# Kernel tuning notes

Hardware: AMD Instinct MI355X
Metric: run time of the kernel (lower is better)

The kernel has to match this reference:

```python
import jax, jax.numpy as jnp
import numpy as np

G = 8          # GroupNorm groups
EPS = 1e-5
L = 4          # num_layers
C = 64         # hidden_channels
CIN = 2        # in_channels


def group_norm(x, gamma, beta):
    B, Cc, H, W = x.shape
    xr = x.reshape(B, G, Cc // G, H, W)
    mu = xr.mean(axis=(2, 3, 4), keepdims=True)
    var = xr.var(axis=(2, 3, 4), keepdims=True)
    xn = ((xr - mu) * jax.lax.rsqrt(var + EPS)).reshape(B, Cc, H, W)
    return xn * gamma[:, None, None] + beta[:, None, None]


def conv1x1(x, w, b):
    # x: [B,Ci,H,W], w: [Co,Ci] -> [B,Co,H,W]
    return jnp.einsum('bchw,oc->bohw', x, w) + b[None, :, None, None]


def conv3x3(x, w, b):
    y = jax.lax.conv_general_dilated(x, w, (1, 1), 'SAME',
                                     dimension_numbers=('NCHW', 'OIHW', 'NCHW'))
    return y + b[None, :, None, None]


def setup_inputs() -> dict:
    key = jax.random.key(0)
    ks = jax.random.split(key, 20)
    s = 0.05
    inp = {
        'x': jax.random.normal(ks[0], (2, CIN, 256, 256), jnp.float32),
        'hidden': jnp.zeros((2, L, C, C), jnp.float32),
        'W_in': jax.random.normal(ks[1], (C, CIN, 3, 3), jnp.float32) * s,
        'b_in': jnp.zeros((C,), jnp.float32),
        'gamma': jnp.ones((L, C), jnp.float32),
        'beta': jnp.zeros((L, C), jnp.float32),
        'Wq': jax.random.normal(ks[2], (L, C, C), jnp.float32) * s,
        'bq': jnp.zeros((L, C), jnp.float32),
        'Wk': jax.random.normal(ks[3], (L, C, C), jnp.float32) * s,
        'bk': jnp.zeros((L, C), jnp.float32),
        'Wv': jax.random.normal(ks[4], (L, C, C), jnp.float32) * s,
        'bv': jnp.zeros((L, C), jnp.float32),
        'Wg': jax.random.normal(ks[5], (L, 2 * C, C), jnp.float32) * s,
        'bg': jnp.zeros((L, 2 * C), jnp.float32),
        'Wp': jax.random.normal(ks[6], (L, C, C), jnp.float32) * s,
        'bp': jnp.zeros((L, C), jnp.float32),
        'W_out': jax.random.normal(ks[7], (CIN, C, 3, 3), jnp.float32) * s,
        'b_out': jnp.zeros((CIN,), jnp.float32),
    }
    return inp


def gla_layer(feat, prev_mem, gamma, beta, Wq, bq, Wk, bk, Wv, bv, Wg, bg, Wp, bp):
    B, Cc, H, W = feat.shape
    N = H * W
    scale = Cc ** (-0.5)
    xn = group_norm(feat, gamma, beta)
    q = conv1x1(xn, Wq, bq).reshape(B, Cc, N) * scale
    k = conv1x1(xn, Wk, bk).reshape(B, Cc, N)
    v = conv1x1(xn, Wv, bv).reshape(B, Cc, N)
    gates = conv1x1(xn, Wg, bg).reshape(B, 2 * Cc, N)
    f_gate = jax.nn.sigmoid(gates[:, :Cc])
    i_gate = jax.nn.sigmoid(gates[:, Cc:])
    k_gated = k * i_gate
    new_knowledge = jnp.einsum('bcn,bdn->bcd', k_gated, v) / N  # [B,C,C]
    global_forget = f_gate.mean(axis=2)[:, :, None]              # [B,C,1]
    new_mem = global_forget * prev_mem + new_knowledge
    retrieved = jnp.einsum('bcn,bcd->bdn', q, new_mem).reshape(B, Cc, H, W)
    out = conv1x1(retrieved, Wp, bp) + feat
    return out, new_mem


def reference(x, hidden, W_in, b_in, gamma, beta, Wq, bq, Wk, bk, Wv, bv,
              Wg, bg, Wp, bp, W_out, b_out):
    feat = conv3x3(x, W_in, b_in)
    mems = []
    for i in range(L):
        feat, m = gla_layer(feat, hidden[:, i], gamma[i], beta[i],
                            Wq[i], bq[i], Wk[i], bk[i], Wv[i], bv[i],
                            Wg[i], bg[i], Wp[i], bp[i])
        mems.append(m)
    new_hidden = jnp.stack(mems, axis=1)  # [B,L,C,C]
    out = conv3x3(feat, W_out, b_out) + x
    return out, new_hidden
```

## Files before the change

### kernel.cpp

```cpp
#include <hip/hip_runtime.h>
#include <hip/hip_bf16.h>

typedef __hip_bfloat16 bf16;
typedef __attribute__((ext_vector_type(8))) short bf16x8;
typedef __attribute__((ext_vector_type(4))) short short4v;
typedef __attribute__((ext_vector_type(4))) float f32x4;

#define BATCH 2
#define CH 64
#define NPIX 65536
#define HDIM 256
#define NLAYER 4
#define NGRP 8
#define NSLOT 512

#define OFS_FEAT   0ull
#define OFS_KSLOT  16777216ull
#define OFS_MEMBG  25165824ull
#define OFS_FSUM   25182208ull
#define OFS_SSUM   25198592ull
#define OFS_BEFF   25214976ull
#define OFS_MEFFB  25215488ull
#define OFS_WKB    25231872ull
#define OFS_WVB    25264640ull
#define OFS_WGB    25297408ull
#define OFS_WTOUT  25362944ull
#define OFS_WPB    25367552ull
#define OFS_WQTB   25400320ull
#define ZERO_BYTES 32768

__device__ __forceinline__ float sigmoidf_(float x){ return 1.0f/(1.0f+__expf(-x)); }

__device__ __forceinline__ short f2bs(float x){
  unsigned u = __float_as_uint(x);
  u += 0x7fffu + ((u >> 16) & 1u);
  return (short)(u >> 16);
}
__device__ __forceinline__ float bs2f(short x){
  return __uint_as_float(((unsigned)(unsigned short)x) << 16);
}

__device__ __forceinline__ float waveReduce(float v){
  #pragma unroll
  for (int off=32; off; off>>=1) v += __shfl_xor(v, off, 64);
  return v;
}

__global__ void k_prepw(const float* __restrict__ Wk, const float* __restrict__ Wv,
                        const float* __restrict__ Wg, const float* __restrict__ Wout,
                        const float* __restrict__ Wp, const float* __restrict__ Wq,
                        short* __restrict__ Wkb, short* __restrict__ Wvb,
                        short* __restrict__ Wgb, float* __restrict__ wtout,
                        short* __restrict__ Wpb, short* __restrict__ Wqtb){
  int i = blockIdx.x*256 + threadIdx.x;
  if (i < 16384){
    Wkb[i] = f2bs(Wk[i]);
    Wvb[i] = f2bs(Wv[i]);
    Wpb[i] = f2bs(Wp[i]);
    int l = i >> 12, within = i & 4095;
    int e = within >> 6, c = within & 63;
    Wqtb[i] = f2bs(Wq[l*4096 + c*64 + e]);
  }
  if (i < 32768) Wgb[i] = f2bs(Wg[i]);
  if (i < 1152){
    int o = i / 576, rem = i % 576;
    int k = rem >> 6, c = rem & 63;
    wtout[(o*9 + k)*64 + c] = Wout[o*576 + c*9 + k];
  }
}

__device__ __forceinline__ void blockStats(const float* gs, const float* gq,
                                           float* ssum_b, int t){
  __shared__ float sacc[16];
  if (t < 16) sacc[t] = 0.f;
  __syncthreads();
  #pragma unroll
  for (int g=0; g<NGRP; g++){
    float s  = waveReduce(gs[g]);
    float sq = waveReduce(gq[g]);
    if ((t & 63) == 0){ atomicAdd(&sacc[g*2], s); atomicAdd(&sacc[g*2+1], sq); }
  }
  __syncthreads();
  if (t < 16) atomicAdd(&ssum_b[t*32], sacc[t]);
}

__global__ void k_conv_in(const float* __restrict__ x, const float* __restrict__ w,
                          const float* __restrict__ bias,
                          short* __restrict__ feat, float* __restrict__ ssum){
  int b = blockIdx.y;
  int t = threadIdx.x;
  int n = blockIdx.x*256 + t;
  int y = n >> 8, xx = n & 255;
  float patch[18];
  int idx = 0;
  #pragma unroll
  for (int ci=0; ci<2; ci++)
    #pragma unroll
    for (int dy=-1; dy<=1; dy++)
      #pragma unroll
      for (int dx=-1; dx<=1; dx++){
        int yy = y+dy, xc = xx+dx;
        float v = 0.f;
        if (yy>=0 && yy<HDIM && xc>=0 && xc<HDIM)
          v = x[((b*2+ci)*HDIM + yy)*HDIM + xc];
        patch[idx++] = v;
      }
  float gs[NGRP], gq[NGRP];
  #pragma unroll
  for (int g=0; g<NGRP; g++){ gs[g]=0.f; gq[g]=0.f; }
  short* fb = feat + ((size_t)b*NPIX + n)*64;
  #pragma unroll
  for (int c4=0; c4<16; c4++){
    short4v sv;
    #pragma unroll
    for (int j=0;j<4;j++){
      int o = c4*4 + j;
      float acc = bias[o];
      #pragma unroll
      for (int k=0; k<18; k++) acc += w[o*18+k]*patch[k];
      sv[j] = f2bs(acc);
      gs[o>>3] += acc; gq[o>>3] += acc*acc;
    }
    *(short4v*)(fb + c4*4) = sv;
  }
  blockStats(gs, gq, ssum + b*512, t);
}

__device__ __forceinline__ void gnCoef(const float* __restrict__ ssum_l, int b, int t,
                                       const float* __restrict__ gammaP,
                                       const float* __restrict__ betaP, int l,
                                       float* s_gnA, float* s_gnB){
  if (t < 64){
    int g = t >> 3;
    const float inv = 1.0f/(8.0f*NPIX);
    float s  = ssum_l[(b*16 + g*2)*32];
    float sq = ssum_l[(b*16 + g*2 + 1)*32];
    float mu = s*inv;
    float var = sq*inv - mu*mu;
    float rstd = rsqrtf(var + 1e-5f);
    float A = rstd * gammaP[l*64 + t];
    s_gnA[t] = A;
    s_gnB[t] = betaP[l*64 + t] - mu * A;
  }
}

__global__ __launch_bounds__(256,3) void k_qkvg_know(
    const short* __restrict__ feat, const float* __restrict__ ssum_l,
    const float* __restrict__ gammaP, const float* __restrict__ betaP,
    const short* __restrict__ Wkb, const float* __restrict__ bkP,
    const short* __restrict__ Wvb, const float* __restrict__ bvP,
    const short* __restrict__ Wgb, const float* __restrict__ bgP,
    int l, short* __restrict__ kslot, float* __restrict__ f_sum)
{
  int b = blockIdx.y;
  int n0 = blockIdx.x * 128;
  int t = threadIdx.x;
  int w = t >> 6;
  int lane = t & 63;
  int m = lane & 15;
  int quad = lane >> 4;
  int rowbase = w*16;

  __shared__ short s_buf[17408];
  short* s_kg = s_buf;
  short* s_v  = s_buf + 8704;
  short* s_xn = s_buf;
  __shared__ float s_gnA[64], s_gnB[64];

  gnCoef(ssum_l, b, t, gammaP, betaP, l, s_gnA, s_gnB);

  float bkv[4], biv[4], bvv[4], bfv[4], fs[4];
  #pragma unroll
  for (int r=0;r<4;r++){
    int row = rowbase + quad*4 + r;
    bkv[r] = bkP[l*64 + row];
    biv[r] = bgP[l*128 + 64 + row];
    bvv[r] = bvP[l*64 + row];
    bfv[r] = bgP[l*128 + row];
    fs[r] = 0.f;
  }
  f32x4 z4 = {0.f,0.f,0.f,0.f};
  f32x4 accn[4];
  #pragma unroll
  for (int dt=0;dt<4;dt++) accn[dt] = z4;

  __syncthreads();

  const short* fbase = feat + ((size_t)b*NPIX + n0)*64;
  #pragma unroll
  for (int i=0;i<4;i++){
    int chunk = t + i*256;
    int px = chunk >> 3, c8 = (chunk & 7)*8;
    bf16x8 rv = *(const bf16x8*)(fbase + px*64 + c8);
    short4v lo, hi;
    #pragma unroll
    for (int j=0;j<4;j++)
      lo[j] = f2bs(fmaf(bs2f(rv[j]), s_gnA[c8+j], s_gnB[c8+j]));
    #pragma unroll
    for (int j=0;j<4;j++)
      hi[j] = f2bs(fmaf(bs2f(rv[j+4]), s_gnA[c8+4+j], s_gnB[c8+4+j]));
    *(short4v*)&s_xn[px*72 + c8]     = lo;
    *(short4v*)&s_xn[px*72 + c8 + 4] = hi;
  }
  __syncthreads();

  bf16x8 Bf[2][8];
  #pragma unroll
  for (int kc=0;kc<2;kc++)
    #pragma unroll
    for (int nt=0;nt<8;nt++)
      Bf[kc][nt] = *(const bf16x8*)&s_xn[(nt*16+m)*72 + kc*32 + quad*8];
  __syncthreads();

  {
    bf16x8 Ak[2], Ai[2];
    #pragma unroll
    for (int kc=0;kc<2;kc++){
      Ak[kc] = *(const bf16x8*)&Wkb[l*4096 + (rowbase+m)*64 + kc*32 + quad*8];
      Ai[kc] = *(const bf16x8*)&Wgb[l*8192 + (64+rowbase+m)*64 + kc*32 + quad*8];
    }
    #pragma unroll
    for (int half=0; half<2; half++){
      f32x4 acck[4], acci[4];
      #pragma unroll
      for (int q4=0;q4<4;q4++){ acck[q4]=z4; acci[q4]=z4; }
      #pragma unroll
      for (int kc=0;kc<2;kc++)
        #pragma unroll
        for (int q4=0;q4<4;q4++){
          acck[q4] = __builtin_amdgcn_mfma_f32_16x16x32_bf16(Ak[kc], Bf[kc][half*4+q4], acck[q4], 0,0,0);
          acci[q4] = __builtin_amdgcn_mfma_f32_16x16x32_bf16(Ai[kc], Bf[kc][half*4+q4], acci[q4], 0,0,0);
        }
      #pragma unroll
      for (int q4=0;q4<4;q4++){
        int nt = half*4+q4;
        #pragma unroll
        for (int r=0;r<4;r++){
          int row = rowbase + quad*4 + r;
          float kv = acck[q4][r] + bkv[r];
          float iv = acci[q4][r] + biv[r];
          s_kg[row*136 + nt*16 + m] = f2bs(kv * sigmoidf_(iv));
        }
      }
    }
  }
  {
    bf16x8 Av[2];
    #pragma unroll
    for (int kc=0;kc<2;kc++)
      Av[kc] = *(const bf16x8*)&Wvb[l*4096 + (rowbase+m)*64 + kc*32 + quad*8];
    #pragma unroll
    for (int half=0; half<2; half++){
      f32x4 accv[4];
      #pragma unroll
      for (int q4=0;q4<4;q4++) accv[q4]=z4;
      #pragma unroll
      for (int kc=0;kc<2;kc++)
        #pragma unroll
        for (int q4=0;q4<4;q4++)
          accv[q4] = __builtin_amdgcn_mfma_f32_16x16x32_bf16(Av[kc], Bf[kc][half*4+q4], accv[q4], 0,0,0);
      #pragma unroll
      for (int q4=0;q4<4;q4++){
        int nt = half*4+q4;
        #pragma unroll
        for (int r=0;r<4;r++){
          int row = rowbase + quad*4 + r;
          s_v[row*136 + nt*16 + m] = f2bs(accv[q4][r] + bvv[r]);
        }
      }
    }
  }
  {
    bf16x8 Af[2];
    #pragma unroll
    for (int kc=0;kc<2;kc++)
      Af[kc] = *(const bf16x8*)&Wgb[l*8192 + (rowbase+m)*64 + kc*32 + quad*8];
    #pragma unroll
    for (int half=0; half<2; half++){
      f32x4 accf[4];
      #pragma unroll
      for (int q4=0;q4<4;q4++) accf[q4]=z4;
      #pragma unroll
      for (int kc=0;kc<2;kc++)
        #pragma unroll
        for (int q4=0;q4<4;q4++)
          accf[q4] = __builtin_amdgcn_mfma_f32_16x16x32_bf16(Af[kc], Bf[kc][half*4+q4], accf[q4], 0,0,0);
      #pragma unroll
      for (int q4=0;q4<4;q4++)
        #pragma unroll
        for (int r=0;r<4;r++)
          fs[r] += sigmoidf_(accf[q4][r] + bfv[r]);
    }
  }
  __syncthreads();

  #pragma unroll
  for (int kc4=0; kc4<4; kc4++){
    bf16x8 a = *(const bf16x8*)&s_kg[(rowbase + m)*136 + kc4*32 + quad*8];
    #pragma unroll
    for (int dt=0; dt<4; dt++){
      bf16x8 bv8 = *(const bf16x8*)&s_v[(dt*16 + m)*136 + kc4*32 + quad*8];
      accn[dt] = __builtin_amdgcn_mfma_f32_16x16x32_bf16(a, bv8, accn[dt], 0,0,0);
    }
  }

  #pragma unroll
  for (int off=1; off<16; off<<=1)
    #pragma unroll
    for (int r=0;r<4;r++) fs[r] += __shfl_xor(fs[r], off, 64);
  if (m == 0){
    #pragma unroll
    for (int r=0;r<4;r++)
      atomicAdd(&f_sum[(b*64 + rowbase + quad*4 + r)*32], fs[r]);
  }
  short* kr = kslot + ((size_t)b*NSLOT + blockIdx.x)*4096;
  #pragma unroll
  for (int dt=0;dt<4;dt++)
    #pragma unroll
    for (int r=0;r<4;r++)
      kr[(rowbase + quad*4 + r)*64 + dt*16 + m] = f2bs(accn[dt][r]);
}

__global__ __launch_bounds__(256) void k_memreduce(
    const short* __restrict__ kslot, const float* __restrict__ f_sum,
    const float* __restrict__ hidden_in, int l,
    float* __restrict__ hidden_out, short* __restrict__ membG)
{
  int b = blockIdx.y;
  int t = threadIdx.x;
  int e = t & 127;
  int half = t >> 7;
  int cd = blockIdx.x*128 + e;

  const short* base = kslot + ((size_t)b*NSLOT + half*256)*4096 + cd;
  float s = 0.f;
  #pragma unroll 16
  for (int sl=0; sl<256; sl++) s += bs2f(base[(size_t)sl*4096]);

  __shared__ float red[128];
  if (half) red[e] = s;
  __syncthreads();
  if (!half){
    const float invN = 1.0f/(float)NPIX;
    float kn = (s + red[e]) * invN;
    float fmean = f_sum[(b*64 + (cd>>6))*32] * invN;
    float pm = hidden_in[(size_t)(b*NLAYER+l)*4096 + cd];
    float nm = fmean*pm + kn;
    hidden_out[(size_t)(b*NLAYER+l)*4096 + cd] = nm;
    membG[b*4096 + cd] = f2bs(nm);
  }
}

__global__ __launch_bounds__(256) void k_meff(
    const short* __restrict__ membG, float* __restrict__ f_sum,
    const short* __restrict__ Wpb, const short* __restrict__ Wqtb,
    const float* __restrict__ bqP, const float* __restrict__ bpP,
    int l, short* __restrict__ Meffb, float* __restrict__ beff,
    float* __restrict__ ssum_next)
{
  int b = blockIdx.x;
  int t = threadIdx.x;
  int w = t >> 6;
  int lane = t & 63;
  int m = lane & 15;
  int quad = lane >> 4;

  __shared__ short s_memb[64*72];
  __shared__ short s_mfb[64*72];
  __shared__ float s_bq[64];

  if (t < 64) s_bq[t] = bqP[l*64 + t];

  #pragma unroll
  for (int i=0;i<16;i++){
    int cd = t + i*256;
    int c = cd >> 6, d = cd & 63;
    s_memb[c*72 + d] = membG[b*4096 + cd];
  }
  __syncthreads();
  if (t < 64) f_sum[(b*64 + t)*32] = 0.f;
  if (t < 16) ssum_next[(b*16 + t)*32] = 0.f;

  f32x4 z4 = {0.f,0.f,0.f,0.f};

  bf16x8 Ap[2];
  #pragma unroll
  for (int kc=0;kc<2;kc++)
    Ap[kc] = *(const bf16x8*)&Wpb[l*4096 + (w*16+m)*64 + kc*32 + quad*8];

  float be[4];
  #pragma unroll
  for (int r=0;r<4;r++) be[r] = 0.f;

  #pragma unroll
  for (int ct=0; ct<4; ct++){
    f32x4 a = z4;
    #pragma unroll
    for (int kc=0;kc<2;kc++){
      bf16x8 Bm = *(const bf16x8*)&s_memb[(ct*16+m)*72 + kc*32 + quad*8];
      a = __builtin_amdgcn_mfma_f32_16x16x32_bf16(Ap[kc], Bm, a, 0,0,0);
    }
    int c = ct*16 + m;
    #pragma unroll
    for (int r=0;r<4;r++){
      int o = w*16 + quad*4 + r;
      s_mfb[o*72 + c] = f2bs(a[r]);
      be[r] += a[r] * s_bq[c];
    }
  }
  #pragma unroll
  for (int off=1; off<16; off<<=1)
    #pragma unroll
    for (int r=0;r<4;r++) be[r] += __shfl_xor(be[r], off, 64);
  if (m == 0){
    #pragma unroll
    for (int r=0;r<4;r++){
      int o = w*16 + quad*4 + r;
      beff[b*64 + o] = bpP[l*64 + o] + 0.125f*be[r];
    }
  }
  __syncthreads();

  bf16x8 Am2[2];
  #pragma unroll
  for (int kc=0;kc<2;kc++)
    Am2[kc] = *(const bf16x8*)&s_mfb[(w*16+m)*72 + kc*32 + quad*8];
  #pragma unroll
  for (int et=0; et<4; et++){
    f32x4 a = z4;
    #pragma unroll
    for (int kc=0;kc<2;kc++){
      bf16x8 Bq = *(const bf16x8*)&Wqtb[l*4096 + (et*16+m)*64 + kc*32 + quad*8];
      a = __builtin_amdgcn_mfma_f32_16x16x32_bf16(Am2[kc], Bq, a, 0,0,0);
    }
    #pragma unroll
    for (int r=0;r<4;r++){
      int o = w*16 + quad*4 + r;
      Meffb[(size_t)b*4096 + o*64 + et*16 + m] = f2bs(0.125f*a[r]);
    }
  }
}

__global__ __launch_bounds__(256,3) void k_retrproj(
    const float* __restrict__ ssum_l,
    const float* __restrict__ gammaP, const float* __restrict__ betaP,
    const short* __restrict__ Meffb, const float* __restrict__ beff,
    int l, short* __restrict__ feat, float* __restrict__ ssum_next)
{
  int b = blockIdx.y;
  int n0 = blockIdx.x * 128;
  int t = threadIdx.x;
  int w = t >> 6;
  int lane = t & 63;
  int m = lane & 15;
  int quad = lane >> 4;

  __shared__ float s_out[128*68];
  short* s_xn = (short*)s_out;
  __shared__ float s_gnA[64], s_gnB[64], s_beff[64];
  __shared__ float s_sacc[16];

  gnCoef(ssum_l, b, t, gammaP, betaP, l, s_gnA, s_gnB);
  if (t < 64) s_beff[t] = beff[b*64 + t];
  if (t < 16) s_sacc[t] = 0.f;
  __syncthreads();

  short* fbase = feat + ((size_t)b*NPIX + n0)*64;
  #pragma unroll
  for (int i=0;i<4;i++){
    int chunk = t + i*256;
    int px = chunk >> 3, c8 = (chunk & 7)*8;
    bf16x8 rv = *(const bf16x8*)(fbase + px*64 + c8);
    short4v lo, hi;
    #pragma unroll
    for (int j=0;j<4;j++)
      lo[j] = f2bs(fmaf(bs2f(rv[j]), s_gnA[c8+j], s_gnB[c8+j]));
    #pragma unroll
    for (int j=0;j<4;j++)
      hi[j] = f2bs(fmaf(bs2f(rv[j+4]), s_gnA[c8+4+j], s_gnB[c8+4+j]));
    *(short4v*)&s_xn[px*72 + c8]     = lo;
    *(short4v*)&s_xn[px*72 + c8 + 4] = hi;
  }
  __syncthreads();

  bf16x8 Bf[2][8];
  #pragma unroll
  for (int kc=0;kc<2;kc++)
    #pragma unroll
    for (int nt=0;nt<8;nt++)
      Bf[kc][nt] = *(const bf16x8*)&s_xn[(nt*16+m)*72 + kc*32 + quad*8];

  bf16x8 Am[2];
  #pragma unroll
  for (int kc=0;kc<2;kc++)
    Am[kc] = *(const bf16x8*)&Meffb[(size_t)b*4096 + (w*16 + m)*64 + kc*32 + quad*8];
  __syncthreads();

  f32x4 acc[8];
  f32x4 z4 = {0.f,0.f,0.f,0.f};
  #pragma unroll
  for (int nt=0;nt<8;nt++) acc[nt]=z4;
  #pragma unroll
  for (int kc=0;kc<2;kc++)
    #pragma unroll
    for (int nt=0;nt<8;nt++)
      acc[nt] = __builtin_amdgcn_mfma_f32_16x16x32_bf16(Am[kc], Bf[kc][nt], acc[nt], 0,0,0);

  #pragma unroll
  for (int nt=0;nt<8;nt++)
    #pragma unroll
    for (int r=0;r<4;r++)
      s_out[(nt*16+m)*68 + w*16 + quad*4 + r] = acc[nt][r];
  __syncthreads();

  float gsv = 0.f, gqv = 0.f;
  int c8 = (t & 7)*8;
  #pragma unroll
  for (int i=0;i<4;i++){
    int chunk = t + i*256;
    int px = chunk >> 3;
    short* fp = fbase + px*64 + c8;
    bf16x8 rv = *(const bf16x8*)fp;
    f32x4 o1 = *(const f32x4*)&s_out[px*68 + c8];
    f32x4 o2 = *(const f32x4*)&s_out[px*68 + c8 + 4];
    short4v r1, r2;
    #pragma unroll
    for (int j=0;j<4;j++){
      float o = bs2f(rv[j]) + o1[j] + s_beff[c8+j];
      r1[j] = f2bs(o);
      gsv += o; gqv += o*o;
    }
    #pragma unroll
    for (int j=0;j<4;j++){
      float o = bs2f(rv[j+4]) + o2[j] + s_beff[c8+4+j];
      r2[j] = f2bs(o);
      gsv += o; gqv += o*o;
    }
    *(short4v*)fp = r1;
    *(short4v*)(fp+4) = r2;
  }
  gsv += __shfl_xor(gsv, 8, 64);  gqv += __shfl_xor(gqv, 8, 64);
  gsv += __shfl_xor(gsv, 16, 64); gqv += __shfl_xor(gqv, 16, 64);
  gsv += __shfl_xor(gsv, 32, 64); gqv += __shfl_xor(gqv, 32, 64);
  if ((lane & 56) == 0){
    int g = lane & 7;
    atomicAdd(&s_sacc[g*2], gsv);
    atomicAdd(&s_sacc[g*2+1], gqv);
  }
  __syncthreads();
  if (t < 16) atomicAdd(&ssum_next[(b*16 + t)*32], s_sacc[t]);
}

__global__ void k_conv_out(const short* __restrict__ feat, const float* __restrict__ wt,
                           const float* __restrict__ bias,
                           const float* __restrict__ xin, float* __restrict__ out){
  int b = blockIdx.y;
  int y = blockIdx.x;
  int xx = threadIdx.x;
  float acc0 = bias[0], acc1 = bias[1];
  #pragma unroll
  for (int dy=-1; dy<=1; dy++){
    int yy = y + dy;
    if (yy < 0 || yy >= HDIM) continue;
    #pragma unroll
    for (int dx=-1; dx<=1; dx++){
      int xc = xx + dx;
      if (xc >= 0 && xc < HDIM){
        const short* fp = feat + ((size_t)b*NPIX + yy*HDIM + xc)*64;
        const float* w0 = wt + ((0*3 + dy+1)*3 + dx+1)*64;
        const float* w1 = wt + ((1*3 + dy+1)*3 + dx+1)*64;
        #pragma unroll
        for (int c8=0;c8<8;c8++){
          bf16x8 fv = *(const bf16x8*)(fp + c8*8);
          f32x4 w0a = *(const f32x4*)(w0 + c8*8);
          f32x4 w0b = *(const f32x4*)(w0 + c8*8 + 4);
          f32x4 w1a = *(const f32x4*)(w1 + c8*8);
          f32x4 w1b = *(const f32x4*)(w1 + c8*8 + 4);
          #pragma unroll
          for (int j=0;j<4;j++){
            float fa = bs2f(fv[j]), fb2 = bs2f(fv[j+4]);
            acc0 += fa*w0a[j] + fb2*w0b[j];
            acc1 += fa*w1a[j] + fb2*w1b[j];
          }
        }
      }
    }
  }
  size_t p0 = (size_t)(b*2+0)*NPIX + y*HDIM + xx;
  size_t p1 = (size_t)(b*2+1)*NPIX + y*HDIM + xx;
  out[p0] = acc0 + xin[p0];
  out[p1] = acc1 + xin[p1];
}

extern "C" void kernel_launch(void* const* d_in, const int* in_sizes, int n_in,
                              void* d_out, int out_size, void* d_ws, size_t ws_size,
                              hipStream_t stream){
  char* ws = (char*)d_ws;
  short* feat  = (short*)(ws + OFS_FEAT);
  short* kslot = (short*)(ws + OFS_KSLOT);
  short* membg = (short*)(ws + OFS_MEMBG);
  float* fsum  = (float*)(ws + OFS_FSUM);
  float* ssum  = (float*)(ws + OFS_SSUM);
  float* beff  = (float*)(ws + OFS_BEFF);
  short* meffb = (short*)(ws + OFS_MEFFB);
  short* wkb   = (short*)(ws + OFS_WKB);
  short* wvb   = (short*)(ws + OFS_WVB);
  short* wgb   = (short*)(ws + OFS_WGB);
  float* wtout = (float*)(ws + OFS_WTOUT);
  short* wpb   = (short*)(ws + OFS_WPB);
  short* wqtb  = (short*)(ws + OFS_WQTB);

  const float* x      = (const float*)d_in[0];
  const float* hidden = (const float*)d_in[1];
  const float* W_in   = (const float*)d_in[2];
  const float* b_in   = (const float*)d_in[3];
  const float* gamma  = (const float*)d_in[4];
  const float* beta   = (const float*)d_in[5];
  const float* Wq     = (const float*)d_in[6];
  const float* bq     = (const float*)d_in[7];
  const float* Wk     = (const float*)d_in[8];
  const float* bk     = (const float*)d_in[9];
  const float* Wv     = (const float*)d_in[10];
  const float* bv     = (const float*)d_in[11];
  const float* Wg     = (const float*)d_in[12];
  const float* bg     = (const float*)d_in[13];
  const float* Wp     = (const float*)d_in[14];
  const float* bp     = (const float*)d_in[15];
  const float* W_out  = (const float*)d_in[16];
  const float* b_out  = (const float*)d_in[17];

  float* out        = (float*)d_out;
  float* hidden_out = out + BATCH*2*NPIX;

  hipMemsetAsync(ws + OFS_FSUM, 0, ZERO_BYTES, stream);
  k_prepw<<<dim3(128), dim3(256), 0, stream>>>(Wk, Wv, Wg, W_out, Wp, Wq,
                                               wkb, wvb, wgb, wtout, wpb, wqtb);
  k_conv_in<<<dim3(HDIM, BATCH), dim3(256), 0, stream>>>(x, W_in, b_in, feat, ssum);

  for (int l=0; l<NLAYER; l++){
    float* ssum_l = ssum + (l & 1)*1024;
    float* ssum_n = ssum + ((l+1) & 1)*1024;
    k_qkvg_know<<<dim3(NPIX/128, BATCH), dim3(256), 0, stream>>>(
        feat, ssum_l, gamma, beta, wkb, bk, wvb, bv, wgb, bg, l, kslot, fsum);
    k_memreduce<<<dim3(32, BATCH), dim3(256), 0, stream>>>(
        kslot, fsum, hidden, l, hidden_out, membg);
    k_meff<<<dim3(BATCH), dim3(256), 0, stream>>>(
        membg, fsum, wpb, wqtb, bq, bp, l, meffb, beff, ssum_n);
    k_retrproj<<<dim3(NPIX/128, BATCH), dim3(256), 0, stream>>>(
        ssum_l, gamma, beta, meffb, beff, l, feat, ssum_n);
  }

  k_conv_out<<<dim3(HDIM, BATCH), dim3(256), 0, stream>>>(feat, wtout, b_out, x, out);
}
```

Before: 358.1 us.

## Fold GroupNorm affine into per-batch 1x1 conv weights and biases

Folds the per-batch GroupNorm scale and shift into the K/I/V/F projection weights and biases (new k_fold kernel per layer) and into the effective retrieval matrix in k_meff. The two large per-pixel kernels can then read raw feat straight into MFMA operands from global memory. This drops the normalize-and-stage pass through LDS and several block barriers. In exchange it adds a small launch per layer, and the bf16 rounding of the folded weights changes numerics slightly.

```diff
diff --git a/kernel.cpp b/kernel.cpp
--- a/kernel.cpp
+++ b/kernel.cpp
@@ -21,12 +21,11 @@
 #define OFS_SSUM   25198592ull
 #define OFS_BEFF   25214976ull
 #define OFS_MEFFB  25215488ull
-#define OFS_WKB    25231872ull
-#define OFS_WVB    25264640ull
-#define OFS_WGB    25297408ull
-#define OFS_WTOUT  25362944ull
-#define OFS_WPB    25367552ull
-#define OFS_WQTB   25400320ull
+#define OFS_WFOLD  25231872ull
+#define OFS_BFOLD  25297408ull
+#define OFS_WTOUT  25299456ull
+#define OFS_WPB    25304064ull
+#define OFS_WQTB   25336832ull
 #define ZERO_BYTES 32768
 
 __device__ __forceinline__ float sigmoidf_(float x){ return 1.0f/(1.0f+__expf(-x)); }
@@ -46,22 +45,17 @@
   return v;
 }
 
-__global__ void k_prepw(const float* __restrict__ Wk, const float* __restrict__ Wv,
-                        const float* __restrict__ Wg, const float* __restrict__ Wout,
-                        const float* __restrict__ Wp, const float* __restrict__ Wq,
-                        short* __restrict__ Wkb, short* __restrict__ Wvb,
-                        short* __restrict__ Wgb, float* __restrict__ wtout,
-                        short* __restrict__ Wpb, short* __restrict__ Wqtb){
+__global__ void k_prepw(const float* __restrict__ Wout, const float* __restrict__ Wp,
+                        const float* __restrict__ Wq,
+                        float* __restrict__ wtout, short* __restrict__ Wpb,
+                        short* __restrict__ Wqtb){
   int i = blockIdx.x*256 + threadIdx.x;
   if (i < 16384){
-    Wkb[i] = f2bs(Wk[i]);
-    Wvb[i] = f2bs(Wv[i]);
     Wpb[i] = f2bs(Wp[i]);
     int l = i >> 12, within = i & 4095;
     int e = within >> 6, c = within & 63;
     Wqtb[i] = f2bs(Wq[l*4096 + c*64 + e]);
   }
-  if (i < 32768) Wgb[i] = f2bs(Wg[i]);
   if (i < 1152){
     int o = i / 576, rem = i % 576;
     int k = rem >> 6, c = rem & 63;
@@ -144,13 +138,55 @@
   }
 }
 
+__global__ __launch_bounds__(256) void k_fold(
+    const float* __restrict__ Wk, const float* __restrict__ Wv,
+    const float* __restrict__ Wg,
+    const float* __restrict__ bkP, const float* __restrict__ bvP,
+    const float* __restrict__ bgP,
+    const float* __restrict__ gammaP, const float* __restrict__ betaP,
+    const float* __restrict__ ssum_l, int l,
+    short* __restrict__ wfold, float* __restrict__ bfold)
+{
+  int mat = blockIdx.x & 3;
+  int b = blockIdx.x >> 2;
+  int t = threadIdx.x;
+  __shared__ float sA[64], sB[64];
+  __shared__ float sred[256];
+
+  gnCoef(ssum_l, b, t, gammaP, betaP, l, sA, sB);
+  __syncthreads();
+
+  const float* Wsrc;
+  const float* bsrc;
+  if (mat == 0){ Wsrc = Wk + l*4096;        bsrc = bkP + l*64; }
+  else if (mat == 1){ Wsrc = Wg + l*8192 + 4096; bsrc = bgP + l*128 + 64; }
+  else if (mat == 2){ Wsrc = Wv + l*4096;   bsrc = bvP + l*64; }
+  else { Wsrc = Wg + l*8192;                bsrc = bgP + l*128; }
+  short* Wdst = wfold + mat*8192 + b*4096;
+  float* bdst = bfold + mat*128 + b*64;
+
+  #pragma unroll
+  for (int idx = t; idx < 4096; idx += 256){
+    int c = idx & 63;
+    Wdst[idx] = f2bs(Wsrc[idx] * sA[c]);
+  }
+  int o = t & 63, cq = t >> 6;
+  float p = 0.f;
+  #pragma unroll
+  for (int cc=0; cc<16; cc++){
+    int c = cq*16 + cc;
+    p += Wsrc[o*64 + c] * sB[c];
+  }
+  sred[t] = p;
+  __syncthreads();
+  if (t < 64)
+    bdst[t] = bsrc[t] + sred[t] + sred[64+t] + sred[128+t] + sred[192+t];
+}
+
 __global__ __launch_bounds__(256,3) void k_qkvg_know(
-    const short* __restrict__ feat, const float* __restrict__ ssum_l,
-    const float* __restrict__ gammaP, const float* __restrict__ betaP,
-    const short* __restrict__ Wkb, const float* __restrict__ bkP,
-    const short* __restrict__ Wvb, const float* __restrict__ bvP,
-    const short* __restrict__ Wgb, const float* __restrict__ bgP,
-    int l, short* __restrict__ kslot, float* __restrict__ f_sum)
+    const short* __restrict__ feat,
+    const short* __restrict__ wfold, const float* __restrict__ bfold,
+    short* __restrict__ kslot, float* __restrict__ f_sum)
 {
   int b = blockIdx.y;
   int n0 = blockIdx.x * 128;
@@ -164,19 +200,20 @@
   __shared__ short s_buf[17408];
   short* s_kg = s_buf;
   short* s_v  = s_buf + 8704;
-  short* s_xn = s_buf;
-  __shared__ float s_gnA[64], s_gnB[64];
-
-  gnCoef(ssum_l, b, t, gammaP, betaP, l, s_gnA, s_gnB);
+
+  const short* wkf = wfold + b*4096;
+  const short* wif = wfold + 8192  + b*4096;
+  const short* wvf = wfold + 16384 + b*4096;
+  const short* wff = wfold + 24576 + b*4096;
 
   float bkv[4], biv[4], bvv[4], bfv[4], fs[4];
   #pragma unroll
   for (int r=0;r<4;r++){
     int row = rowbase + quad*4 + r;
-    bkv[r] = bkP[l*64 + row];
-    biv[r] = bgP[l*128 + 64 + row];
-    bvv[r] = bvP[l*64 + row];
-    bfv[r] = bgP[l*128 + row];
+    bkv[r] = bfold[b*64 + row];
+    biv[r] = bfold[128 + b*64 + row];
+    bvv[r] = bfold[256 + b*64 + row];
+    bfv[r] = bfold[384 + b*64 + row];
     fs[r] = 0.f;
   }
   f32x4 z4 = {0.f,0.f,0.f,0.f};
@@ -184,40 +221,20 @@
   #pragma unroll
   for (int dt=0;dt<4;dt++) accn[dt] = z4;
 
-  __syncthreads();
-
   const short* fbase = feat + ((size_t)b*NPIX + n0)*64;
-  #pragma unroll
-  for (int i=0;i<4;i++){
-    int chunk = t + i*256;
-    int px = chunk >> 3, c8 = (chunk & 7)*8;
-    bf16x8 rv = *(const bf16x8*)(fbase + px*64 + c8);
-    short4v lo, hi;
-    #pragma unroll
-    for (int j=0;j<4;j++)
-      lo[j] = f2bs(fmaf(bs2f(rv[j]), s_gnA[c8+j], s_gnB[c8+j]));
-    #pragma unroll
-    for (int j=0;j<4;j++)
-      hi[j] = f2bs(fmaf(bs2f(rv[j+4]), s_gnA[c8+4+j], s_gnB[c8+4+j]));
-    *(short4v*)&s_xn[px*72 + c8]     = lo;
-    *(short4v*)&s_xn[px*72 + c8 + 4] = hi;
-  }
-  __syncthreads();
-
   bf16x8 Bf[2][8];
   #pragma unroll
   for (int kc=0;kc<2;kc++)
     #pragma unroll
     for (int nt=0;nt<8;nt++)
-      Bf[kc][nt] = *(const bf16x8*)&s_xn[(nt*16+m)*72 + kc*32 + quad*8];
-  __syncthreads();
+      Bf[kc][nt] = *(const bf16x8*)(fbase + (nt*16+m)*64 + kc*32 + quad*8);
 
   {
     bf16x8 Ak[2], Ai[2];
     #pragma unroll
     for (int kc=0;kc<2;kc++){
-      Ak[kc] = *(const bf16x8*)&Wkb[l*4096 + (rowbase+m)*64 + kc*32 + quad*8];
-      Ai[kc] = *(const bf16x8*)&Wgb[l*8192 + (64+rowbase+m)*64 + kc*32 + quad*8];
+      Ak[kc] = *(const bf16x8*)&wkf[(rowbase+m)*64 + kc*32 + quad*8];
+      Ai[kc] = *(const bf16x8*)&wif[(rowbase+m)*64 + kc*32 + quad*8];
     }
     #pragma unroll
     for (int half=0; half<2; half++){
@@ -248,7 +265,7 @@
     bf16x8 Av[2];
     #pragma unroll
     for (int kc=0;kc<2;kc++)
-      Av[kc] = *(const bf16x8*)&Wvb[l*4096 + (rowbase+m)*64 + kc*32 + quad*8];
+      Av[kc] = *(const bf16x8*)&wvf[(rowbase+m)*64 + kc*32 + quad*8];
     #pragma unroll
     for (int half=0; half<2; half++){
       f32x4 accv[4];
@@ -274,7 +291,7 @@
     bf16x8 Af[2];
     #pragma unroll
     for (int kc=0;kc<2;kc++)
-      Af[kc] = *(const bf16x8*)&Wgb[l*8192 + (rowbase+m)*64 + kc*32 + quad*8];
+      Af[kc] = *(const bf16x8*)&wff[(rowbase+m)*64 + kc*32 + quad*8];
     #pragma unroll
     for (int half=0; half<2; half++){
       f32x4 accf[4];
@@ -355,6 +372,8 @@
     const short* __restrict__ membG, float* __restrict__ f_sum,
     const short* __restrict__ Wpb, const short* __restrict__ Wqtb,
     const float* __restrict__ bqP, const float* __restrict__ bpP,
+    const float* __restrict__ gammaP, const float* __restrict__ betaP,
+    const float* __restrict__ ssum_l,
     int l, short* __restrict__ Meffb, float* __restrict__ beff,
     float* __restrict__ ssum_next)
 {
@@ -367,8 +386,9 @@
 
   __shared__ short s_memb[64*72];
   __shared__ short s_mfb[64*72];
-  __shared__ float s_bq[64];
-
+  __shared__ float s_bq[64], s_A[64], s_B[64];
+
+  gnCoef(ssum_l, b, t, gammaP, betaP, l, s_A, s_B);
   if (t < 64) s_bq[t] = bqP[l*64 + t];
 
   #pragma unroll
@@ -408,6 +428,28 @@
       be[r] += a[r] * s_bq[c];
     }
   }
+  __syncthreads();
+
+  bf16x8 Am2[2];
+  #pragma unroll
+  for (int kc=0;kc<2;kc++)
+    Am2[kc] = *(const bf16x8*)&s_mfb[(w*16+m)*72 + kc*32 + quad*8];
+  #pragma unroll
+  for (int et=0; et<4; et++){
+    f32x4 a = z4;
+    #pragma unroll
+    for (int kc=0;kc<2;kc++){
+      bf16x8 Bq = *(const bf16x8*)&Wqtb[l*4096 + (et*16+m)*64 + kc*32 + quad*8];
+      a = __builtin_amdgcn_mfma_f32_16x16x32_bf16(Am2[kc], Bq, a, 0,0,0);
+    }
+    int e = et*16 + m;
+    #pragma unroll
+    for (int r=0;r<4;r++){
+      int o = w*16 + quad*4 + r;
+      Meffb[(size_t)b*4096 + o*64 + e] = f2bs(0.125f*a[r]*s_A[e]);
+      be[r] += a[r] * s_B[e];
+    }
+  }
   #pragma unroll
   for (int off=1; off<16; off<<=1)
     #pragma unroll
@@ -419,33 +461,11 @@
       beff[b*64 + o] = bpP[l*64 + o] + 0.125f*be[r];
     }
   }
-  __syncthreads();
-
-  bf16x8 Am2[2];
-  #pragma unroll
-  for (int kc=0;kc<2;kc++)
-    Am2[kc] = *(const bf16x8*)&s_mfb[(w*16+m)*72 + kc*32 + quad*8];
-  #pragma unroll
-  for (int et=0; et<4; et++){
-    f32x4 a = z4;
-    #pragma unroll
-    for (int kc=0;kc<2;kc++){
-      bf16x8 Bq = *(const bf16x8*)&Wqtb[l*4096 + (et*16+m)*64 + kc*32 + quad*8];
-      a = __builtin_amdgcn_mfma_f32_16x16x32_bf16(Am2[kc], Bq, a, 0,0,0);
-    }
-    #pragma unroll
-    for (int r=0;r<4;r++){
-      int o = w*16 + quad*4 + r;
-      Meffb[(size_t)b*4096 + o*64 + et*16 + m] = f2bs(0.125f*a[r]);
-    }
-  }
 }
 
 __global__ __launch_bounds__(256,3) void k_retrproj(
-    const float* __restrict__ ssum_l,
-    const float* __restrict__ gammaP, const float* __restrict__ betaP,
     const short* __restrict__ Meffb, const float* __restrict__ beff,
-    int l, short* __restrict__ feat, float* __restrict__ ssum_next)
+    short* __restrict__ feat, float* __restrict__ ssum_next)
 {
   int b = blockIdx.y;
   int n0 = blockIdx.x * 128;
@@ -456,45 +476,25 @@
   int quad = lane >> 4;
 
   __shared__ float s_out[128*68];
-  short* s_xn = (short*)s_out;
-  __shared__ float s_gnA[64], s_gnB[64], s_beff[64];
+  __shared__ float s_beff[64];
   __shared__ float s_sacc[16];
 
-  gnCoef(ssum_l, b, t, gammaP, betaP, l, s_gnA, s_gnB);
   if (t < 64) s_beff[t] = beff[b*64 + t];
   if (t < 16) s_sacc[t] = 0.f;
-  __syncthreads();
 
   short* fbase = feat + ((size_t)b*NPIX + n0)*64;
-  #pragma unroll
-  for (int i=0;i<4;i++){
-    int chunk = t + i*256;
-    int px = chunk >> 3, c8 = (chunk & 7)*8;
-    bf16x8 rv = *(const bf16x8*)(fbase + px*64 + c8);
-    short4v lo, hi;
-    #pragma unroll
-    for (int j=0;j<4;j++)
-      lo[j] = f2bs(fmaf(bs2f(rv[j]), s_gnA[c8+j], s_gnB[c8+j]));
-    #pragma unroll
-    for (int j=0;j<4;j++)
-      hi[j] = f2bs(fmaf(bs2f(rv[j+4]), s_gnA[c8+4+j], s_gnB[c8+4+j]));
-    *(short4v*)&s_xn[px*72 + c8]     = lo;
-    *(short4v*)&s_xn[px*72 + c8 + 4] = hi;
-  }
-  __syncthreads();
 
   bf16x8 Bf[2][8];
   #pragma unroll
   for (int kc=0;kc<2;kc++)
     #pragma unroll
     for (int nt=0;nt<8;nt++)
-      Bf[kc][nt] = *(const bf16x8*)&s_xn[(nt*16+m)*72 + kc*32 + quad*8];
+      Bf[kc][nt] = *(const bf16x8*)(fbase + (nt*16+m)*64 + kc*32 + quad*8);
 
   bf16x8 Am[2];
   #pragma unroll
   for (int kc=0;kc<2;kc++)
     Am[kc] = *(const bf16x8*)&Meffb[(size_t)b*4096 + (w*16 + m)*64 + kc*32 + quad*8];
-  __syncthreads();
 
   f32x4 acc[8];
   f32x4 z4 = {0.f,0.f,0.f,0.f};
@@ -603,9 +603,8 @@
   float* ssum  = (float*)(ws + OFS_SSUM);
   float* beff  = (float*)(ws + OFS_BEFF);
   short* meffb = (short*)(ws + OFS_MEFFB);
-  short* wkb   = (short*)(ws + OFS_WKB);
-  short* wvb   = (short*)(ws + OFS_WVB);
-  short* wgb   = (short*)(ws + OFS_WGB);
+  short* wfold = (short*)(ws + OFS_WFOLD);
+  float* bfold = (float*)(ws + OFS_BFOLD);
   float* wtout = (float*)(ws + OFS_WTOUT);
   short* wpb   = (short*)(ws + OFS_WPB);
   short* wqtb  = (short*)(ws + OFS_WQTB);
@@ -633,21 +632,22 @@
   float* hidden_out = out + BATCH*2*NPIX;
 
   hipMemsetAsync(ws + OFS_FSUM, 0, ZERO_BYTES, stream);
-  k_prepw<<<dim3(128), dim3(256), 0, stream>>>(Wk, Wv, Wg, W_out, Wp, Wq,
-                                               wkb, wvb, wgb, wtout, wpb, wqtb);
+  k_prepw<<<dim3(64), dim3(256), 0, stream>>>(W_out, Wp, Wq, wtout, wpb, wqtb);
   k_conv_in<<<dim3(HDIM, BATCH), dim3(256), 0, stream>>>(x, W_in, b_in, feat, ssum);
 
   for (int l=0; l<NLAYER; l++){
     float* ssum_l = ssum + (l & 1)*1024;
     float* ssum_n = ssum + ((l+1) & 1)*1024;
+    k_fold<<<dim3(8), dim3(256), 0, stream>>>(
+        Wk, Wv, Wg, bk, bv, bg, gamma, beta, ssum_l, l, wfold, bfold);
     k_qkvg_know<<<dim3(NPIX/128, BATCH), dim3(256), 0, stream>>>(
-        feat, ssum_l, gamma, beta, wkb, bk, wvb, bv, wgb, bg, l, kslot, fsum);
+        feat, wfold, bfold, kslot, fsum);
     k_memreduce<<<dim3(32, BATCH), dim3(256), 0, stream>>>(
         kslot, fsum, hidden, l, hidden_out, membg);
     k_meff<<<dim3(BATCH), dim3(256), 0, stream>>>(
-        membg, fsum, wpb, wqtb, bq, bp, l, meffb, beff, ssum_n);
+        membg, fsum, wpb, wqtb, bq, bp, gamma, beta, ssum_l, l, meffb, beff, ssum_n);
     k_retrproj<<<dim3(NPIX/128, BATCH), dim3(256), 0, stream>>>(
-        ssum_l, gamma, beta, meffb, beff, l, feat, ssum_n);
+        meffb, beff, feat, ssum_n);
   }
 
   k_conv_out<<<dim3(HDIM, BATCH), dim3(256), 0, stream>>>(feat, wtout, b_out, x, out);
```

Result: slower. 417.2 us (+16.5%).

## Fold Meff computation into retrproj blocks and drop the k_meff launch

Applied to the files above, without the earlier changes.

Removes the tiny 2-block k_meff kernel. Each k_retrproj block now recomputes the effective matrix Wp·M·Wq^T and the bias from membG in shared memory before its main work. The f_sum and ssum_next zeroing moves into k_memreduce, which now reads fmean before clearing it. This removes one launch and one serialised low-occupancy kernel per layer. In exchange, all 1024 retrproj blocks repeat small MFMA work and extra shared-memory phases.

```diff
diff --git a/kernel.cpp b/kernel.cpp
--- a/kernel.cpp
+++ b/kernel.cpp
@@ -19,14 +19,12 @@
 #define OFS_MEMBG  25165824ull
 #define OFS_FSUM   25182208ull
 #define OFS_SSUM   25198592ull
-#define OFS_BEFF   25214976ull
-#define OFS_MEFFB  25215488ull
-#define OFS_WKB    25231872ull
-#define OFS_WVB    25264640ull
-#define OFS_WGB    25297408ull
-#define OFS_WTOUT  25362944ull
-#define OFS_WPB    25367552ull
-#define OFS_WQTB   25400320ull
+#define OFS_WKB    25214976ull
+#define OFS_WVB    25247744ull
+#define OFS_WGB    25280512ull
+#define OFS_WTOUT  25346048ull
+#define OFS_WPB    25350656ull
+#define OFS_WQTB   25383424ull
 #define ZERO_BYTES 32768
 
 __device__ __forceinline__ float sigmoidf_(float x){ return 1.0f/(1.0f+__expf(-x)); }
@@ -322,9 +320,10 @@
 }
 
 __global__ __launch_bounds__(256) void k_memreduce(
-    const short* __restrict__ kslot, const float* __restrict__ f_sum,
+    const short* __restrict__ kslot, float* __restrict__ f_sum,
     const float* __restrict__ hidden_in, int l,
-    float* __restrict__ hidden_out, short* __restrict__ membG)
+    float* __restrict__ hidden_out, short* __restrict__ membG,
+    float* __restrict__ ssum_next)
 {
   int b = blockIdx.y;
   int t = threadIdx.x;
@@ -332,6 +331,9 @@
   int half = t >> 7;
   int cd = blockIdx.x*128 + e;
 
+  const float invN = 1.0f/(float)NPIX;
+  float fmean = f_sum[(b*64 + (cd>>6))*32] * invN;
+
   const short* base = kslot + ((size_t)b*NSLOT + half*256)*4096 + cd;
   float s = 0.f;
   #pragma unroll 16
@@ -341,110 +343,23 @@
   if (half) red[e] = s;
   __syncthreads();
   if (!half){
-    const float invN = 1.0f/(float)NPIX;
     float kn = (s + red[e]) * invN;
-    float fmean = f_sum[(b*64 + (cd>>6))*32] * invN;
     float pm = hidden_in[(size_t)(b*NLAYER+l)*4096 + cd];
     float nm = fmean*pm + kn;
     hidden_out[(size_t)(b*NLAYER+l)*4096 + cd] = nm;
     membG[b*4096 + cd] = f2bs(nm);
-  }
-}
-
-__global__ __launch_bounds__(256) void k_meff(
-    const short* __restrict__ membG, float* __restrict__ f_sum,
-    const short* __restrict__ Wpb, const short* __restrict__ Wqtb,
-    const float* __restrict__ bqP, const float* __restrict__ bpP,
-    int l, short* __restrict__ Meffb, float* __restrict__ beff,
-    float* __restrict__ ssum_next)
-{
-  int b = blockIdx.x;
-  int t = threadIdx.x;
-  int w = t >> 6;
-  int lane = t & 63;
-  int m = lane & 15;
-  int quad = lane >> 4;
-
-  __shared__ short s_memb[64*72];
-  __shared__ short s_mfb[64*72];
-  __shared__ float s_bq[64];
-
-  if (t < 64) s_bq[t] = bqP[l*64 + t];
-
-  #pragma unroll
-  for (int i=0;i<16;i++){
-    int cd = t + i*256;
-    int c = cd >> 6, d = cd & 63;
-    s_memb[c*72 + d] = membG[b*4096 + cd];
-  }
-  __syncthreads();
-  if (t < 64) f_sum[(b*64 + t)*32] = 0.f;
-  if (t < 16) ssum_next[(b*16 + t)*32] = 0.f;
-
-  f32x4 z4 = {0.f,0.f,0.f,0.f};
-
-  bf16x8 Ap[2];
-  #pragma unroll
-  for (int kc=0;kc<2;kc++)
-    Ap[kc] = *(const bf16x8*)&Wpb[l*4096 + (w*16+m)*64 + kc*32 + quad*8];
-
-  float be[4];
-  #pragma unroll
-  for (int r=0;r<4;r++) be[r] = 0.f;
-
-  #pragma unroll
-  for (int ct=0; ct<4; ct++){
-    f32x4 a = z4;
-    #pragma unroll
-    for (int kc=0;kc<2;kc++){
-      bf16x8 Bm = *(const bf16x8*)&s_memb[(ct*16+m)*72 + kc*32 + quad*8];
-      a = __builtin_amdgcn_mfma_f32_16x16x32_bf16(Ap[kc], Bm, a, 0,0,0);
-    }
-    int c = ct*16 + m;
-    #pragma unroll
-    for (int r=0;r<4;r++){
-      int o = w*16 + quad*4 + r;
-      s_mfb[o*72 + c] = f2bs(a[r]);
-      be[r] += a[r] * s_bq[c];
-    }
-  }
-  #pragma unroll
-  for (int off=1; off<16; off<<=1)
-    #pragma unroll
-    for (int r=0;r<4;r++) be[r] += __shfl_xor(be[r], off, 64);
-  if (m == 0){
-    #pragma unroll
-    for (int r=0;r<4;r++){
-      int o = w*16 + quad*4 + r;
-      beff[b*64 + o] = bpP[l*64 + o] + 0.125f*be[r];
-    }
-  }
-  __syncthreads();
-
-  bf16x8 Am2[2];
-  #pragma unroll
-  for (int kc=0;kc<2;kc++)
-    Am2[kc] = *(const bf16x8*)&s_mfb[(w*16+m)*72 + kc*32 + quad*8];
-  #pragma unroll
-  for (int et=0; et<4; et++){
-    f32x4 a = z4;
-    #pragma unroll
-    for (int kc=0;kc<2;kc++){
-      bf16x8 Bq = *(const bf16x8*)&Wqtb[l*4096 + (et*16+m)*64 + kc*32 + quad*8];
-      a = __builtin_amdgcn_mfma_f32_16x16x32_bf16(Am2[kc], Bq, a, 0,0,0);
-    }
-    #pragma unroll
-    for (int r=0;r<4;r++){
-      int o = w*16 + quad*4 + r;
-      Meffb[(size_t)b*4096 + o*64 + et*16 + m] = f2bs(0.125f*a[r]);
-    }
-  }
+  } else {
+    if ((e & 63) == 0) f_sum[(b*64 + (cd>>6))*32] = 0.f;
+  }
+  if (blockIdx.x == 0 && t < 16) ssum_next[(b*16 + t)*32] = 0.f;
 }
 
 __global__ __launch_bounds__(256,3) void k_retrproj(
     const float* __restrict__ ssum_l,
     const float* __restrict__ gammaP, const float* __restrict__ betaP,
-    const short* __restrict__ Meffb, const float* __restrict__ beff,
+    const short* __restrict__ membG,
+    const short* __restrict__ Wpb, const short* __restrict__ Wqtb,
+    const float* __restrict__ bqP, const float* __restrict__ bpP,
     int l, short* __restrict__ feat, float* __restrict__ ssum_next)
 {
   int b = blockIdx.y;
@@ -456,13 +371,89 @@
   int quad = lane >> 4;
 
   __shared__ float s_out[128*68];
-  short* s_xn = (short*)s_out;
-  __shared__ float s_gnA[64], s_gnB[64], s_beff[64];
+  short* s_memb = (short*)s_out;
+  short* s_mfb  = (short*)s_out + 4608;
+  short* s_meff = (short*)s_out;
+  short* s_xn   = (short*)s_out;
+  __shared__ float s_gnA[64], s_gnB[64], s_beff[64], s_bq[64];
   __shared__ float s_sacc[16];
 
   gnCoef(ssum_l, b, t, gammaP, betaP, l, s_gnA, s_gnB);
-  if (t < 64) s_beff[t] = beff[b*64 + t];
+  if (t < 64) s_bq[t] = bqP[l*64 + t];
   if (t < 16) s_sacc[t] = 0.f;
+
+  #pragma unroll
+  for (int i=0;i<16;i++){
+    int cd = t + i*256;
+    int c = cd >> 6, d = cd & 63;
+    s_memb[c*72 + d] = membG[b*4096 + cd];
+  }
+  __syncthreads();
+
+  f32x4 z4 = {0.f,0.f,0.f,0.f};
+
+  bf16x8 Ap[2];
+  #pragma unroll
+  for (int kc=0;kc<2;kc++)
+    Ap[kc] = *(const bf16x8*)&Wpb[l*4096 + (w*16+m)*64 + kc*32 + quad*8];
+
+  float be[4];
+  #pragma unroll
+  for (int r=0;r<4;r++) be[r] = 0.f;
+
+  #pragma unroll
+  for (int ct=0; ct<4; ct++){
+    f32x4 a = z4;
+    #pragma unroll
+    for (int kc=0;kc<2;kc++){
+      bf16x8 Bm = *(const bf16x8*)&s_memb[(ct*16+m)*72 + kc*32 + quad*8];
+      a = __builtin_amdgcn_mfma_f32_16x16x32_bf16(Ap[kc], Bm, a, 0,0,0);
+    }
+    int c = ct*16 + m;
+    #pragma unroll
+    for (int r=0;r<4;r++){
+      int o = w*16 + quad*4 + r;
+      s_mfb[o*72 + c] = f2bs(a[r]);
+      be[r] += a[r] * s_bq[c];
+    }
+  }
+  __syncthreads();
+
+  bf16x8 Am2[2];
+  #pragma unroll
+  for (int kc=0;kc<2;kc++)
+    Am2[kc] = *(const bf16x8*)&s_mfb[(w*16+m)*72 + kc*32 + quad*8];
+  #pragma unroll
+  for (int et=0; et<4; et++){
+    f32x4 a = z4;
+    #pragma unroll
+    for (int kc=0;kc<2;kc++){
+      bf16x8 Bq = *(const bf16x8*)&Wqtb[l*4096 + (et*16+m)*64 + kc*32 + quad*8];
+      a = __builtin_amdgcn_mfma_f32_16x16x32_bf16(Am2[kc], Bq, a, 0,0,0);
+    }
+    #pragma unroll
+    for (int r=0;r<4;r++){
+      int o = w*16 + quad*4 + r;
+      s_meff[o*72 + et*16 + m] = f2bs(0.125f*a[r]);
+    }
+  }
+  #pragma unroll
+  for (int off=1; off<16; off<<=1)
+    #pragma unroll
+    for (int r=0;r<4;r++) be[r] += __shfl_xor(be[r], off, 64);
+  if (m == 0){
+    #pragma unroll
+    for (int r=0;r<4;r++){
+      int o = w*16 + quad*4 + r;
+      s_beff[o] = bpP[l*64 + o] + 0.125f*be[r];
+    }
+  }
+  __syncthreads();
+
+  bf16x8 Am[2];
+  #pragma unroll
+  for (int kc=0;kc<2;kc++)
+    Am[kc] = *(const bf16x8*)&s_meff[(w*16 + m)*72 + kc*32 + quad*8];
   __syncthreads();
 
   short* fbase = feat + ((size_t)b*NPIX + n0)*64;
@@ -489,15 +480,9 @@
     #pragma unroll
     for (int nt=0;nt<8;nt++)
       Bf[kc][nt] = *(const bf16x8*)&s_xn[(nt*16+m)*72 + kc*32 + quad*8];
-
-  bf16x8 Am[2];
-  #pragma unroll
-  for (int kc=0;kc<2;kc++)
-    Am[kc] = *(const bf16x8*)&Meffb[(size_t)b*4096 + (w*16 + m)*64 + kc*32 + quad*8];
   __syncthreads();
 
   f32x4 acc[8];
-  f32x4 z4 = {0.f,0.f,0.f,0.f};
   #pragma unroll
   for (int nt=0;nt<8;nt++) acc[nt]=z4;
   #pragma unroll
@@ -601,8 +586,6 @@
   short* membg = (short*)(ws + OFS_MEMBG);
   float* fsum  = (float*)(ws + OFS_FSUM);
   float* ssum  = (float*)(ws + OFS_SSUM);
-  float* beff  = (float*)(ws + OFS_BEFF);
-  short* meffb = (short*)(ws + OFS_MEFFB);
   short* wkb   = (short*)(ws + OFS_WKB);
   short* wvb   = (short*)(ws + OFS_WVB);
   short* wgb   = (short*)(ws + OFS_WGB);
@@ -643,11 +626,9 @@
     k_qkvg_know<<<dim3(NPIX/128, BATCH), dim3(256), 0, stream>>>(
         feat, ssum_l, gamma, beta, wkb, bk, wvb, bv, wgb, bg, l, kslot, fsum);
     k_memreduce<<<dim3(32, BATCH), dim3(256), 0, stream>>>(
-        kslot, fsum, hidden, l, hidden_out, membg);
-    k_meff<<<dim3(BATCH), dim3(256), 0, stream>>>(
-        membg, fsum, wpb, wqtb, bq, bp, l, meffb, beff, ssum_n);
+        kslot, fsum, hidden, l, hidden_out, membg, ssum_n);
     k_retrproj<<<dim3(NPIX/128, BATCH), dim3(256), 0, stream>>>(
-        ssum_l, gamma, beta, meffb, beff, l, feat, ssum_n);
+        ssum_l, gamma, beta, membg, wpb, wqtb, bq, bp, l, feat, ssum_n);
   }
 
   k_conv_out<<<dim3(HDIM, BATCH), dim3(256), 0, stream>>>(feat, wtout, b_out, x, out);
```

New measurement: 372.4 us. 4.0% more time.
